# Kernel tuning notes

Hardware: AMD Instinct MI355X
Metric: run time of the kernel (lower is better)

Reference implementation:

```python
import jax, jax.numpy as jnp
import numpy as np

NEG_SLOPE = 0.01  # torch F.leaky_relu default

N_NODES = 100000
N_EDGES = 1250000
N_REL = 10
D = 64


def setup_inputs() -> dict:
    key = jax.random.key(0)
    ks = jax.random.split(key, 8)
    return {
        "nfeat": jax.random.normal(ks[0], (N_NODES, D), dtype=jnp.float32),
        "efeat": jax.random.normal(ks[1], (N_EDGES, D), dtype=jnp.float32),
        "relation_weight": jax.random.normal(ks[2], (N_REL, D, D), dtype=jnp.float32) * (1.0 / np.sqrt(D)),
        "res_fc_w": jax.random.normal(ks[3], (D, D), dtype=jnp.float32) * (1.0 / np.sqrt(D)),
        "res_fc2_w": jax.random.normal(ks[4], (D, D), dtype=jnp.float32) * (1.0 / np.sqrt(D)),
        "src": jax.random.randint(ks[5], (N_EDGES,), 0, N_NODES, dtype=jnp.int32),
        "dst": jnp.sort(jax.random.randint(ks[6], (N_EDGES,), 0, N_NODES, dtype=jnp.int32)),
        "etype": jax.random.randint(ks[7], (N_EDGES,), 0, N_REL, dtype=jnp.int32),
    }


def reference(nfeat, efeat, relation_weight, res_fc_w, res_fc2_w, src, dst, etype):
    # KGAT conv (eval mode, feat_drop=0):
    #   t_r = W_{r(e)} h_src,  h_r = W_{r(e)} h_dst
    #   att = <t_r, tanh(h_r + e_r)>  per edge
    #   a   = edge_softmax over incoming edges of dst
    #   h_neighbor[v] = sum_{e: dst=v} a_e * h_src
    #   h' = leaky_relu((h + h_nb) W1^T) + leaky_relu((h * h_nb) W2^T)
    n = nfeat.shape[0]
    # Project every node by every relation once (N*R*D), instead of
    # materializing a per-edge [E, D, D] weight gather.
    proj = jnp.einsum('ni,rio->nro', nfeat, relation_weight)  # [N, R, D]
    t_r = proj[src, etype]   # [E, D]
    h_r = proj[dst, etype]   # [E, D]
    att = jnp.sum(t_r * jnp.tanh(h_r + efeat), axis=-1)  # [E]

    # segment softmax over dst (edge_softmax)
    seg_max = jax.ops.segment_max(att, dst, num_segments=n)  # [N]
    ex = jnp.exp(att - seg_max[dst])
    seg_sum = jax.ops.segment_sum(ex, dst, num_segments=n)   # [N]
    a = ex / seg_sum[dst]                                    # [E]

    # weighted scatter-sum aggregation of src features
    h_nb = jax.ops.segment_sum(nfeat[src] * a[:, None], dst, num_segments=n)  # [N, D]

    out = (jax.nn.leaky_relu((nfeat + h_nb) @ res_fc_w.T, NEG_SLOPE)
           + jax.nn.leaky_relu((nfeat * h_nb) @ res_fc2_w.T, NEG_SLOPE))
    return out
```

## Files before the change

kernel.cpp:

```cpp
#include <hip/hip_runtime.h>
#include <hip/hip_fp16.h>
#include <math.h>

#define D 64
#define WAVE 64

__device__ __forceinline__ float wave_reduce_sum(float v) {
    v += __shfl_xor(v, 32);
    v += __shfl_xor(v, 16);
    v += __shfl_xor(v, 8);
    v += __shfl_xor(v, 4);
    v += __shfl_xor(v, 2);
    v += __shfl_xor(v, 1);
    return v;
}

__device__ __forceinline__ float wave_reduce_max(float v) {
    v = fmaxf(v, __shfl_xor(v, 32));
    v = fmaxf(v, __shfl_xor(v, 16));
    v = fmaxf(v, __shfl_xor(v, 8));
    v = fmaxf(v, __shfl_xor(v, 4));
    v = fmaxf(v, __shfl_xor(v, 2));
    v = fmaxf(v, __shfl_xor(v, 1));
    return v;
}

__device__ __forceinline__ float fast_tanh(float x) {
    float e = __expf(2.0f * x);
    return 1.0f - 2.0f / (e + 1.0f);
}

__global__ __launch_bounds__(256) void proj_kernel(
    const float* __restrict__ nfeat, const float* __restrict__ W,
    __half* __restrict__ proj, int n_nodes, int n_rel, int nodes_per_block) {
    const int lane = threadIdx.x & 63;
    const int wid = __builtin_amdgcn_readfirstlane(threadIdx.x >> 6);
    const int r = blockIdx.y;

    float w[D];
    const float* Wr = W + (size_t)r * D * D;
#pragma unroll
    for (int i = 0; i < D; ++i) w[i] = Wr[i * D + lane];

    int n0 = blockIdx.x * nodes_per_block;
    int n1 = n0 + nodes_per_block;
    if (n1 > n_nodes) n1 = n_nodes;
    for (int n = n0 + wid; n < n1; n += 4) {
        const int nn = __builtin_amdgcn_readfirstlane(n);
        const float* __restrict__ x = nfeat + (size_t)nn * D;
        float a0 = 0.0f, a1 = 0.0f, a2 = 0.0f, a3 = 0.0f;
#pragma unroll
        for (int i = 0; i < D; i += 4) {
            a0 = fmaf(x[i + 0], w[i + 0], a0);
            a1 = fmaf(x[i + 1], w[i + 1], a1);
            a2 = fmaf(x[i + 2], w[i + 2], a2);
            a3 = fmaf(x[i + 3], w[i + 3], a3);
        }
        proj[((size_t)nn * n_rel + r) * D + lane] = __float2half_rn((a0 + a1) + (a2 + a3));
    }
}

__global__ __launch_bounds__(256) void att_kernel(
    const __half* __restrict__ proj, const float* __restrict__ efeat,
    const int* __restrict__ src, const int* __restrict__ dst,
    const int* __restrict__ etype, float* __restrict__ att,
    int n_edges, int n_rel) {
    const int lane = threadIdx.x & 63;
    const int wid = threadIdx.x >> 6;
    const int g = lane >> 4;
    const int c4 = lane & 15;

    int e = (blockIdx.x * 4 + wid) * 4 + g;
    const bool valid = e < n_edges;
    const int ec = valid ? e : (n_edges - 1);
    const int s = src[ec];
    const int d = dst[ec];
    const int et = etype[ec];

    const float4* ef4 = (const float4*)(efeat + (size_t)ec * D);
    float4 ef = ef4[c4];
    const __half2* tp = (const __half2*)(proj + ((size_t)s * n_rel + et) * D) + c4 * 2;
    const __half2* hp = (const __half2*)(proj + ((size_t)d * n_rel + et) * D) + c4 * 2;
    float2 tA = __half22float2(tp[0]);
    float2 tB = __half22float2(tp[1]);
    float2 hA = __half22float2(hp[0]);
    float2 hB = __half22float2(hp[1]);

    float v = tA.x * fast_tanh(hA.x + ef.x)
            + tA.y * fast_tanh(hA.y + ef.y)
            + tB.x * fast_tanh(hB.x + ef.z)
            + tB.y * fast_tanh(hB.y + ef.w);
    v += __shfl_xor(v, 8);
    v += __shfl_xor(v, 4);
    v += __shfl_xor(v, 2);
    v += __shfl_xor(v, 1);
    if (valid && c4 == 0) att[e] = v;
}

__global__ void rowptr_kernel(const int* __restrict__ dst, int* __restrict__ row_ptr,
                              int n_edges, int n_nodes) {
    int tid = blockIdx.x * blockDim.x + threadIdx.x;
    int stride = gridDim.x * blockDim.x;
    for (int e = tid; e < n_edges; e += stride) {
        int d = dst[e];
        int dprev = (e == 0) ? -1 : dst[e - 1];
        for (int v = dprev + 1; v <= d; ++v) row_ptr[v] = e;
    }
    if (tid == 0) {
        int dlast = dst[n_edges - 1];
        for (int v = dlast + 1; v <= n_nodes; ++v) row_ptr[v] = n_edges;
    }
}

__global__ __launch_bounds__(256) void agg_kernel(
    const float* __restrict__ att, const int* __restrict__ src,
    const int* __restrict__ row_ptr, const float* __restrict__ nfeat,
    float* __restrict__ h_nb, int n_nodes) {
    const int lane = threadIdx.x & 63;
    const int wid = __builtin_amdgcn_readfirstlane(threadIdx.x >> 6);
    const int n = blockIdx.x * 4 + wid;
    if (n >= n_nodes) return;
    const int s = row_ptr[n];
    const int t = row_ptr[n + 1];
    float a0 = 0.0f, a1 = 0.0f, a2 = 0.0f, a3 = 0.0f;
    float inv = 0.0f;
    if (t > s) {
        float m = -INFINITY;
        for (int base = s; base < t; base += WAVE) {
            int idx = base + lane;
            float a = (idx < t) ? att[idx] : -INFINITY;
            m = fmaxf(m, a);
        }
        m = wave_reduce_max(m);
        float exsum = 0.0f;
        for (int base = s; base < t; base += WAVE) {
            int idx = base + lane;
            float ex = (idx < t) ? __expf(att[idx] - m) : 0.0f;
            int sv = (idx < t) ? src[idx] : 0;
            exsum += ex;
            int cnt = t - base;
            if (cnt > WAVE) cnt = WAVE;
            int cnt4 = (cnt + 3) & ~3;
            for (int j = 0; j < cnt4; j += 4) {
                float c0 = __shfl(ex, j + 0); int s0 = __shfl(sv, j + 0);
                float c1 = __shfl(ex, j + 1); int s1 = __shfl(sv, j + 1);
                float c2 = __shfl(ex, j + 2); int s2 = __shfl(sv, j + 2);
                float c3 = __shfl(ex, j + 3); int s3 = __shfl(sv, j + 3);
                a0 = fmaf(c0, nfeat[(size_t)s0 * D + lane], a0);
                a1 = fmaf(c1, nfeat[(size_t)s1 * D + lane], a1);
                a2 = fmaf(c2, nfeat[(size_t)s2 * D + lane], a2);
                a3 = fmaf(c3, nfeat[(size_t)s3 * D + lane], a3);
            }
        }
        float ssum = wave_reduce_sum(exsum);
        inv = 1.0f / ssum;
    }
    h_nb[(size_t)n * D + lane] = ((a0 + a1) + (a2 + a3)) * inv;
}

__global__ __launch_bounds__(256) void out_kernel(
    const float* __restrict__ nfeat, const float* h_nb,
    const float* __restrict__ W1, const float* __restrict__ W2,
    float* out, int n_nodes) {
    const int lane = threadIdx.x & 63;
    const int wid = __builtin_amdgcn_readfirstlane(threadIdx.x >> 6);
    float w1[D], w2[D];
#pragma unroll
    for (int i = 0; i < D; ++i) w1[i] = W1[lane * D + i];
#pragma unroll
    for (int i = 0; i < D; ++i) w2[i] = W2[lane * D + i];
    const int nwaves = gridDim.x * 4;
    for (int n = blockIdx.x * 4 + wid; n < n_nodes; n += nwaves) {
        const int nn = __builtin_amdgcn_readfirstlane(n);
        const float* x = nfeat + (size_t)nn * D;
        const float* h = h_nb + (size_t)nn * D;
        float a0 = 0.0f, a1 = 0.0f, b0 = 0.0f, b1 = 0.0f;
#pragma unroll
        for (int i = 0; i < D; i += 2) {
            float x0 = x[i], h0 = h[i];
            float x1 = x[i + 1], h1 = h[i + 1];
            a0 = fmaf(x0 + h0, w1[i], a0);
            b0 = fmaf(x0 * h0, w2[i], b0);
            a1 = fmaf(x1 + h1, w1[i + 1], a1);
            b1 = fmaf(x1 * h1, w2[i + 1], b1);
        }
        float a = a0 + a1, b = b0 + b1;
        a = (a > 0.0f) ? a : 0.01f * a;
        b = (b > 0.0f) ? b : 0.01f * b;
        out[(size_t)nn * D + lane] = a + b;
    }
}

extern "C" void kernel_launch(void* const* d_in, const int* in_sizes, int n_in,
                              void* d_out, int out_size, void* d_ws, size_t ws_size,
                              hipStream_t stream) {
    const float* nfeat = (const float*)d_in[0];
    const float* efeat = (const float*)d_in[1];
    const float* relw  = (const float*)d_in[2];
    const float* w1    = (const float*)d_in[3];
    const float* w2    = (const float*)d_in[4];
    const int*   src   = (const int*)d_in[5];
    const int*   dst   = (const int*)d_in[6];
    const int*   etype = (const int*)d_in[7];
    float* out = (float*)d_out;

    const int n_nodes = in_sizes[0] / D;
    const int n_edges = in_sizes[5];
    const int n_rel   = in_sizes[2] / (D * D);

    const size_t ALIGN = 256;
    const size_t proj_bytes = ((size_t)n_nodes * n_rel * D * sizeof(__half) + ALIGN - 1) & ~(ALIGN - 1);
    const size_t att_bytes  = ((size_t)n_edges * sizeof(float) + ALIGN - 1) & ~(ALIGN - 1);

    float* h_nb = out;

    char* ws = (char*)d_ws;
    __half* proj  = (__half*)ws;
    float* att    = (float*)(ws + proj_bytes);
    int* row_ptr  = (int*)(ws + proj_bytes + att_bytes);

    rowptr_kernel<<<1024, 256, 0, stream>>>(dst, row_ptr, n_edges, n_nodes);

    const int NODES_PER_BLOCK = 256;
    dim3 pgrid((n_nodes + NODES_PER_BLOCK - 1) / NODES_PER_BLOCK, n_rel);
    proj_kernel<<<pgrid, 256, 0, stream>>>(nfeat, relw, proj, n_nodes, n_rel, NODES_PER_BLOCK);

    att_kernel<<<(n_edges + 15) / 16, 256, 0, stream>>>(proj, efeat, src, dst, etype,
                                                        att, n_edges, n_rel);

    agg_kernel<<<(n_nodes + 3) / 4, 256, 0, stream>>>(att, src, row_ptr, nfeat,
                                                      h_nb, n_nodes);

    out_kernel<<<1024, 256, 0, stream>>>(nfeat, h_nb, w1, w2, out, n_nodes);
}
```

Measured before the change: 846.6 us.

## Tile node features in LDS and loop over relations inside proj kernel

The projection kernel now stages a tile of 128 node feature rows into shared memory once per block and loops over all relations inside the block, reloading each relation's weight column into registers. Previously each (node block, relation) pair reread the node features from global memory. This cuts repeated global reads of nfeat by the relation count, at the cost of fewer blocks (no relation grid dimension), a 32KB LDS allocation and serial per-relation weight reloads.

```diff
diff --git a/kernel.cpp b/kernel.cpp
--- a/kernel.cpp
+++ b/kernel.cpp
@@ -4,6 +4,7 @@
 
 #define D 64
 #define WAVE 64
+#define TILE 128
 
 __device__ __forceinline__ float wave_reduce_sum(float v) {
     v += __shfl_xor(v, 32);
@@ -32,31 +33,46 @@
 
 __global__ __launch_bounds__(256) void proj_kernel(
     const float* __restrict__ nfeat, const float* __restrict__ W,
-    __half* __restrict__ proj, int n_nodes, int n_rel, int nodes_per_block) {
-    const int lane = threadIdx.x & 63;
-    const int wid = __builtin_amdgcn_readfirstlane(threadIdx.x >> 6);
-    const int r = blockIdx.y;
-
-    float w[D];
-    const float* Wr = W + (size_t)r * D * D;
-#pragma unroll
-    for (int i = 0; i < D; ++i) w[i] = Wr[i * D + lane];
-
-    int n0 = blockIdx.x * nodes_per_block;
-    int n1 = n0 + nodes_per_block;
-    if (n1 > n_nodes) n1 = n_nodes;
-    for (int n = n0 + wid; n < n1; n += 4) {
-        const int nn = __builtin_amdgcn_readfirstlane(n);
-        const float* __restrict__ x = nfeat + (size_t)nn * D;
-        float a0 = 0.0f, a1 = 0.0f, a2 = 0.0f, a3 = 0.0f;
-#pragma unroll
-        for (int i = 0; i < D; i += 4) {
-            a0 = fmaf(x[i + 0], w[i + 0], a0);
-            a1 = fmaf(x[i + 1], w[i + 1], a1);
-            a2 = fmaf(x[i + 2], w[i + 2], a2);
-            a3 = fmaf(x[i + 3], w[i + 3], a3);
-        }
-        proj[((size_t)nn * n_rel + r) * D + lane] = __float2half_rn((a0 + a1) + (a2 + a3));
+    __half* __restrict__ proj, int n_nodes, int n_rel) {
+    __shared__ float xs[TILE][D];
+    const int tid = threadIdx.x;
+    const int lane = tid & 63;
+    const int wid = tid >> 6;
+    const int n0 = blockIdx.x * TILE;
+
+    const float4* g4 = (const float4*)(nfeat + (size_t)n0 * D);
+    float4* s4 = (float4*)(&xs[0][0]);
+    int avail_rows = n_nodes - n0;
+    if (avail_rows > TILE) avail_rows = TILE;
+    const int avail4 = avail_rows * (D / 4);
+#pragma unroll
+    for (int i = tid; i < TILE * (D / 4); i += 256) {
+        s4[i] = (i < avail4) ? g4[i] : make_float4(0.f, 0.f, 0.f, 0.f);
+    }
+    __syncthreads();
+
+    const int nloc0 = wid * (TILE / 4);
+    for (int r = 0; r < n_rel; ++r) {
+        float w[D];
+        const float* Wr = W + (size_t)r * D * D;
+#pragma unroll
+        for (int i = 0; i < D; ++i) w[i] = Wr[i * D + lane];
+        for (int k = 0; k < TILE / 4; ++k) {
+            const int n = n0 + nloc0 + k;
+            if (n >= n_nodes) break;
+            const float4* x4 = (const float4*)(&xs[nloc0 + k][0]);
+            float a0 = 0.f, a1 = 0.f, a2 = 0.f, a3 = 0.f;
+#pragma unroll
+            for (int i = 0; i < D / 4; ++i) {
+                float4 xv = x4[i];
+                a0 = fmaf(xv.x, w[4 * i + 0], a0);
+                a1 = fmaf(xv.y, w[4 * i + 1], a1);
+                a2 = fmaf(xv.z, w[4 * i + 2], a2);
+                a3 = fmaf(xv.w, w[4 * i + 3], a3);
+            }
+            proj[((size_t)n * n_rel + r) * D + lane] =
+                __float2half_rn((a0 + a1) + (a2 + a3));
+        }
     }
 }
 
@@ -221,9 +237,8 @@
 
     rowptr_kernel<<<1024, 256, 0, stream>>>(dst, row_ptr, n_edges, n_nodes);
 
-    const int NODES_PER_BLOCK = 256;
-    dim3 pgrid((n_nodes + NODES_PER_BLOCK - 1) / NODES_PER_BLOCK, n_rel);
-    proj_kernel<<<pgrid, 256, 0, stream>>>(nfeat, relw, proj, n_nodes, n_rel, NODES_PER_BLOCK);
+    proj_kernel<<<(n_nodes + TILE - 1) / TILE, 256, 0, stream>>>(
+        nfeat, relw, proj, n_nodes, n_rel);
 
     att_kernel<<<(n_edges + 15) / 16, 256, 0, stream>>>(proj, efeat, src, dst, etype,
                                                         att, n_edges, n_rel);
```

New measurement: 869.8 us. 2.7% more time.
